# Performance work log

Hardware: AMD Instinct MI355X
Metric: run time of the kernel (lower is better)

The kernel has to match this reference:

```python
import jax, jax.numpy as jnp
import numpy as np

N, C, H, W = 32, 512, 32, 32
K = 64  # num_clusters
D_OUT = 256


def _l2n(v, axis):
    # torch F.normalize: v / max(||v||, 1e-12)
    n = jnp.linalg.norm(v, axis=axis, keepdims=True)
    return v / jnp.maximum(n, 1e-12)


def _bn(v, gamma, beta):
    # BatchNorm1d, training mode (batch stats, biased variance), eps=1e-5
    m = v.mean(axis=0)
    var = ((v - m) ** 2).mean(axis=0)
    return (v - m) / jnp.sqrt(var + 1e-5) * gamma + beta


def setup_inputs() -> dict:
    key = jax.random.key(0)
    ks = jax.random.split(key, 5)
    x = jax.random.normal(ks[0], (N, C, H, W), dtype=jnp.float32)
    conv_w = jax.random.normal(ks[1], (K, C), dtype=jnp.float32) * 0.05
    centroids = jax.random.uniform(ks[2], (K, C), dtype=jnp.float32)
    hidden_w = jax.random.normal(ks[3], (K * C, D_OUT), dtype=jnp.float32) / jnp.sqrt(jnp.float32(C))
    gating_w = jax.random.normal(ks[4], (D_OUT, D_OUT), dtype=jnp.float32) / jnp.sqrt(jnp.float32(D_OUT))
    return {
        "x": x,
        "conv_w": conv_w,
        "centroids": centroids,
        "hidden_w": hidden_w,
        "bn2_gamma": jnp.ones((D_OUT,), jnp.float32),
        "bn2_beta": jnp.zeros((D_OUT,), jnp.float32),
        "gating_w": gating_w,
        "gbn_gamma": jnp.ones((D_OUT,), jnp.float32),
        "gbn_beta": jnp.zeros((D_OUT,), jnp.float32),
    }


def reference(x, conv_w, centroids, hidden_w, bn2_gamma, bn2_beta, gating_w, gbn_gamma, gbn_beta):
    n = x.shape[0]
    # descriptor-wise L2 normalization over channel dim
    x = _l2n(x, axis=1)                                  # [N,C,H,W]
    xf = x.reshape(n, x.shape[1], -1)                    # [N,C,S]
    # 1x1 conv -> soft assignment, softmax over clusters
    sa = jnp.einsum('ncs,kc->nks', xf, conv_w)           # [N,K,S]
    sa = jax.nn.softmax(sa, axis=1)
    # matmul-form NetVLAD: sum_s a[n,k,s]*(x[n,c,s]-cent[k,c])
    vlad = jnp.einsum('nks,ncs->nkc', sa, xf) \
         - sa.sum(axis=-1)[..., None] * centroids[None]  # [N,K,C]
    vlad = _l2n(vlad, axis=2)                            # intra-normalization
    vlad = _l2n(vlad.reshape(n, -1), axis=1)             # [N,K*C]
    v = vlad @ hidden_w                                  # [N,256]
    v = _bn(v, bn2_gamma, bn2_beta)
    # context gating
    gates = jax.nn.sigmoid(_bn(v @ gating_w, gbn_gamma, gbn_beta))
    return v * gates
```

## Files before the change

kernel.cpp:

```cpp
#include <hip/hip_runtime.h>
#include <math.h>

static constexpr int Nb = 32;
static constexpr int Cc = 512;
static constexpr int Ss = 1024;
static constexpr int Kk = 64;
static constexpr int Dd = 256;

typedef __attribute__((ext_vector_type(8))) short bf16x8;
typedef __attribute__((ext_vector_type(4))) float f32x4;
typedef __attribute__((ext_vector_type(4))) unsigned int u32x4;

union FragU { u32x4 u; bf16x8 h; };

__device__ __forceinline__ unsigned hi_pack(float x0, float x1) {
    return __builtin_amdgcn_perm(__float_as_uint(x1), __float_as_uint(x0), 0x07060302u);
}
__device__ __forceinline__ float trunc_hi(float x) {
    return __uint_as_float(__float_as_uint(x) & 0xFFFF0000u);
}
__device__ __forceinline__ void split8(const float* xv, FragU& bh, FragU& bl) {
#pragma unroll
    for (int p = 0; p < 4; ++p) {
        bh.u[p] = hi_pack(xv[2*p], xv[2*p+1]);
        float l0 = xv[2*p]   - trunc_hi(xv[2*p]);
        float l1 = xv[2*p+1] - trunc_hi(xv[2*p+1]);
        bl.u[p] = hi_pack(l0, l1);
    }
}

__global__ __launch_bounds__(256) void kprep_cw(
    const float* __restrict__ cw, short* __restrict__ cwh, short* __restrict__ cwl)
{
    int t = blockIdx.x * 256 + threadIdx.x;
    float4 v = *(const float4*)&cw[4 * (size_t)t];
    unsigned h0 = hi_pack(v.x, v.y), h1 = hi_pack(v.z, v.w);
    float l0 = v.x - trunc_hi(v.x), l1 = v.y - trunc_hi(v.y);
    float l2 = v.z - trunc_hi(v.z), l3 = v.w - trunc_hi(v.w);
    unsigned g0 = hi_pack(l0, l1), g1 = hi_pack(l2, l3);
    ((uint2*)cwh)[t] = make_uint2(h0, h1);
    ((uint2*)cwl)[t] = make_uint2(g0, g1);
}

__global__ __launch_bounds__(512) void k1_sa(
    const float* __restrict__ x, const short* __restrict__ cw_hi,
    const short* __restrict__ cw_lo, short* __restrict__ a_hi,
    short* __restrict__ a_lo, float* __restrict__ asum_part)
{
    __shared__ f32x4 comb[4][64][4];
    __shared__ float combq[4][64];

    const int tid = threadIdx.x;
    const int w = tid >> 6, lane = tid & 63;
    const int wq = w & 3, wh = w >> 2;
    const int l15 = lane & 15, lg = lane >> 4;
    const int n = blockIdx.y, s0 = blockIdx.x * 64;
    const int scol = s0 + 16 * wq + l15;

    f32x4 zero4 = {0.f, 0.f, 0.f, 0.f};
    f32x4 acc[4] = {zero4, zero4, zero4, zero4};
    float ssq = 0.f;

    const float* xcol = x + (size_t)n * Cc * Ss + scol;

#pragma unroll 2
    for (int ct = 0; ct < 8; ++ct) {
        const int cb = wh * 256 + ct * 32 + 8 * lg;
        float xv[8];
#pragma unroll
        for (int j = 0; j < 8; ++j) xv[j] = xcol[(size_t)(cb + j) * Ss];
#pragma unroll
        for (int j = 0; j < 8; ++j) ssq += xv[j] * xv[j];
        FragU bh, bl;
        split8(xv, bh, bl);
#pragma unroll
        for (int m = 0; m < 4; ++m) {
            FragU ah, al;
            const int row = 16 * m + l15;
            ah.u = *(const u32x4*)&cw_hi[(size_t)row * Cc + cb];
            al.u = *(const u32x4*)&cw_lo[(size_t)row * Cc + cb];
            acc[m] = __builtin_amdgcn_mfma_f32_16x16x32_bf16(al.h, bh.h, acc[m], 0, 0, 0);
            acc[m] = __builtin_amdgcn_mfma_f32_16x16x32_bf16(ah.h, bl.h, acc[m], 0, 0, 0);
            acc[m] = __builtin_amdgcn_mfma_f32_16x16x32_bf16(ah.h, bh.h, acc[m], 0, 0, 0);
        }
    }

    if (wh == 1) {
#pragma unroll
        for (int m = 0; m < 4; ++m) comb[wq][lane][m] = acc[m];
        combq[wq][lane] = ssq;
    }
    __syncthreads();
    if (wh == 1) return;

#pragma unroll
    for (int m = 0; m < 4; ++m) acc[m] += comb[wq][lane][m];
    ssq += combq[wq][lane];

    ssq += __shfl_xor(ssq, 16);
    ssq += __shfl_xor(ssq, 32);
    const float inv = 1.f / fmaxf(sqrtf(ssq), 1e-12f);

    float sv[4][4];
    float mmax = -1e30f;
#pragma unroll
    for (int m = 0; m < 4; ++m)
#pragma unroll
        for (int r = 0; r < 4; ++r) {
            sv[m][r] = acc[m][r] * inv;
            mmax = fmaxf(mmax, sv[m][r]);
        }
    mmax = fmaxf(mmax, __shfl_xor(mmax, 16));
    mmax = fmaxf(mmax, __shfl_xor(mmax, 32));
    float den = 0.f;
#pragma unroll
    for (int m = 0; m < 4; ++m)
#pragma unroll
        for (int r = 0; r < 4; ++r) {
            sv[m][r] = expf(sv[m][r] - mmax);
            den += sv[m][r];
        }
    den += __shfl_xor(den, 16);
    den += __shfl_xor(den, 32);
    const float rinv = 1.f / den;

#pragma unroll
    for (int m = 0; m < 4; ++m)
#pragma unroll
        for (int r = 0; r < 4; ++r) {
            const float a = sv[m][r] * rinv;
            const int k = 16 * m + 4 * lg + r;
            float t = a;
            t += __shfl_xor(t, 1); t += __shfl_xor(t, 2);
            t += __shfl_xor(t, 4); t += __shfl_xor(t, 8);
            if (l15 == 0)
                asum_part[((size_t)(n * Kk + k) << 6) + blockIdx.x * 4 + wq] = t;
            const float av = a * inv;
            const unsigned u = __float_as_uint(av);
            const float hv = __uint_as_float(u & 0xFFFF0000u);
            const size_t idx = (size_t)(n * Kk + k) * Ss + scol;
            a_hi[idx] = (short)(u >> 16);
            a_lo[idx] = (short)(__float_as_uint(av - hv) >> 16);
        }
}

__global__ __launch_bounds__(256) void kasum(
    const float* __restrict__ asum_part, float* __restrict__ asum)
{
    int row = blockIdx.x * 256 + threadIdx.x;
    const float* p = &asum_part[(size_t)row << 6];
    float s = 0.f;
#pragma unroll
    for (int i = 0; i < 16; ++i) {
        float4 v = *(const float4*)&p[4 * i];
        s += v.x + v.y + v.z + v.w;
    }
    asum[row] = s;
}

__global__ __launch_bounds__(512) void k2_vlad(
    const float* __restrict__ x, const short* __restrict__ a_hi,
    const short* __restrict__ a_lo, const float* __restrict__ centroids,
    const float* __restrict__ asum, float* __restrict__ vp0,
    float* __restrict__ vp1)
{
    __shared__ f32x4 comb[4][64][4];
    __shared__ float asum_l[64];

    const int tid = threadIdx.x;
    const int w = tid >> 6, lane = tid & 63;
    const int wq = w & 3, wh = w >> 2;
    const int l15 = lane & 15, lg = lane >> 4;
    const int n = blockIdx.x, cp = blockIdx.y, sh = blockIdx.z;

    if (sh == 1 && tid < 64) asum_l[tid] = asum[n * Kk + tid];

    f32x4 zero4 = {0.f, 0.f, 0.f, 0.f};
    f32x4 acc[4] = {zero4, zero4, zero4, zero4};

    const int c = cp * 64 + 16 * wq + l15;
    const int sbase = sh * 512 + wh * 256;
    const float* xrow = x + (size_t)(n * Cc + c) * Ss + sbase;
    const short* ahb = a_hi + (size_t)n * Kk * Ss + sbase;
    const short* alb = a_lo + (size_t)n * Kk * Ss + sbase;

#pragma unroll 2
    for (int st = 0; st < 8; ++st) {
        const int so = st * 32 + 8 * lg;
        float4 xa = *(const float4*)&xrow[so];
        float4 xb = *(const float4*)&xrow[so + 4];
        float xv[8] = {xa.x, xa.y, xa.z, xa.w, xb.x, xb.y, xb.z, xb.w};
        FragU bh, bl;
        split8(xv, bh, bl);
#pragma unroll
        for (int m = 0; m < 4; ++m) {
            FragU ah, al;
            const size_t ao = (size_t)(16 * m + l15) * Ss + so;
            ah.u = *(const u32x4*)&ahb[ao];
            al.u = *(const u32x4*)&alb[ao];
            acc[m] = __builtin_amdgcn_mfma_f32_16x16x32_bf16(al.h, bh.h, acc[m], 0, 0, 0);
            acc[m] = __builtin_amdgcn_mfma_f32_16x16x32_bf16(ah.h, bl.h, acc[m], 0, 0, 0);
            acc[m] = __builtin_amdgcn_mfma_f32_16x16x32_bf16(ah.h, bh.h, acc[m], 0, 0, 0);
        }
    }

    if (wh == 1) {
#pragma unroll
        for (int m = 0; m < 4; ++m) comb[wq][lane][m] = acc[m];
    }
    __syncthreads();
    if (wh == 1) return;

    float* dst = sh ? vp1 : vp0;
#pragma unroll
    for (int m = 0; m < 4; ++m) {
        acc[m] += comb[wq][lane][m];
#pragma unroll
        for (int r = 0; r < 4; ++r) {
            const int k = 16 * m + 4 * lg + r;
            float val = acc[m][r];
            if (sh == 1) val -= asum_l[k] * centroids[(size_t)k * Cc + c];
            dst[(size_t)(n * Kk + k) * Cc + c] = val;
        }
    }
}

__global__ __launch_bounds__(512) void k3a_norm(
    float* __restrict__ vlad, const float* __restrict__ vp1,
    float* __restrict__ nrm)
{
    const int tid = threadIdx.x;
    const int w = tid >> 6, lane = tid & 63;
    const int n = blockIdx.x, kg = blockIdx.y;
    const int row = (n * Kk) + kg * 8 + w;
    const size_t base = (size_t)row * Cc + lane * 8;

    float4 v0 = *(const float4*)&vlad[base];
    float4 v1 = *(const float4*)&vlad[base + 4];
    float4 u0 = *(const float4*)&vp1[base];
    float4 u1 = *(const float4*)&vp1[base + 4];
    v0.x += u0.x; v0.y += u0.y; v0.z += u0.z; v0.w += u0.w;
    v1.x += u1.x; v1.y += u1.y; v1.z += u1.z; v1.w += u1.w;
    *(float4*)&vlad[base] = v0;
    *(float4*)&vlad[base + 4] = v1;
    float ssq = v0.x*v0.x + v0.y*v0.y + v0.z*v0.z + v0.w*v0.w
              + v1.x*v1.x + v1.y*v1.y + v1.z*v1.z + v1.w*v1.w;
#pragma unroll
    for (int off = 32; off >= 1; off >>= 1) ssq += __shfl_xor(ssq, off);
    if (lane == 0) nrm[row] = sqrtf(ssq);
}

__global__ __launch_bounds__(64) void k3b_scale(
    const float* __restrict__ nrm, float* __restrict__ scale)
{
    const int n = blockIdx.x, k = threadIdx.x;
    float r = nrm[n * Kk + k];
    float rn = r / fmaxf(r, 1e-12f);
    float p = rn * rn;
#pragma unroll
    for (int off = 32; off >= 1; off >>= 1) p += __shfl_xor(p, off);
    float g = sqrtf(p);
    scale[n * Kk + k] = 1.f / (fmaxf(r, 1e-12f) * fmaxf(g, 1e-12f));
}

__global__ __launch_bounds__(512) void k4_hidden(
    const float* __restrict__ vlad, const float* __restrict__ scale,
    const float* __restrict__ hw, float* __restrict__ vpart)
{
    __shared__ float vl[128][36];
    __shared__ float scale_l[32];
    const int tid = threadIdx.x;
    const int kc0 = blockIdx.x * 128;
    const int k = kc0 >> 9;
    if (tid < 32) scale_l[tid] = scale[tid * Kk + k];
    __syncthreads();
#pragma unroll
    for (int i = 0; i < 8; ++i) {
        int idx = tid + i * 512;
        int nn = idx >> 7, kcl = idx & 127;
        vl[kcl][nn] = vlad[(size_t)nn * (Kk * Cc) + kc0 + kcl] * scale_l[nn];
    }
    __syncthreads();

    const int dq = tid & 63, nq = tid >> 6;
    float acc[4][4];
#pragma unroll
    for (int i = 0; i < 4; ++i)
#pragma unroll
        for (int j = 0; j < 4; ++j) acc[i][j] = 0.f;

    for (int kcl = 0; kcl < 128; ++kcl) {
        const float4 v0 = *(const float4*)&vl[kcl][nq * 4];
        const float* wrow = &hw[(size_t)(kc0 + kcl) * Dd + dq];
#pragma unroll
        for (int dd = 0; dd < 4; ++dd) {
            float w = wrow[64 * dd];
            acc[dd][0] += w * v0.x; acc[dd][1] += w * v0.y;
            acc[dd][2] += w * v0.z; acc[dd][3] += w * v0.w;
        }
    }
#pragma unroll
    for (int dd = 0; dd < 4; ++dd)
#pragma unroll
        for (int j = 0; j < 4; ++j)
            vpart[((size_t)blockIdx.x * Nb + nq * 4 + j) * Dd + dq + 64 * dd] = acc[dd][j];
}

__global__ __launch_bounds__(128) void k5a_reduce(
    const float* __restrict__ vpart, float* __restrict__ v)
{
    int flat = blockIdx.x * 128 + threadIdx.x;
    float s = 0.f;
#pragma unroll 8
    for (int ch = 0; ch < 256; ++ch) s += vpart[(size_t)ch * (Nb * Dd) + flat];
    v[flat] = s;
}

__global__ __launch_bounds__(256) void k5b_bn(
    const float* __restrict__ v, const float* __restrict__ gamma,
    const float* __restrict__ beta, float* __restrict__ v_bn)
{
    const int d = threadIdx.x;
    float vals[Nb];
    float s1 = 0.f;
#pragma unroll
    for (int n = 0; n < Nb; ++n) {
        vals[n] = v[n * Dd + d];
        s1 += vals[n];
    }
    float m = s1 * (1.f / Nb);
    float var = 0.f;
#pragma unroll
    for (int n = 0; n < Nb; ++n) {
        float t = vals[n] - m;
        var += t * t;
    }
    var *= (1.f / Nb);
    float inv = rsqrtf(var + 1e-5f);
    float g = gamma[d], b = beta[d];
#pragma unroll
    for (int n = 0; n < Nb; ++n)
        v_bn[n * Dd + d] = (vals[n] - m) * inv * g + b;
}

__global__ __launch_bounds__(256) void k5c_gate(
    const float* __restrict__ v_bn, const float* __restrict__ gw,
    float* __restrict__ g_raw)
{
    __shared__ float vb[Dd];
    const int n = blockIdx.x, d = threadIdx.x;
    vb[d] = v_bn[n * Dd + d];
    __syncthreads();
    float acc = 0.f;
#pragma unroll 8
    for (int c = 0; c < Dd; ++c) acc += vb[c] * gw[c * Dd + d];
    g_raw[n * Dd + d] = acc;
}

__global__ __launch_bounds__(256) void k5d_out(
    const float* __restrict__ g_raw, const float* __restrict__ v_bn,
    const float* __restrict__ ggamma, const float* __restrict__ gbeta,
    float* __restrict__ out)
{
    const int d = threadIdx.x;
    float vals[Nb];
    float s1 = 0.f;
#pragma unroll
    for (int n = 0; n < Nb; ++n) {
        vals[n] = g_raw[n * Dd + d];
        s1 += vals[n];
    }
    float m = s1 * (1.f / Nb);
    float var = 0.f;
#pragma unroll
    for (int n = 0; n < Nb; ++n) {
        float t = vals[n] - m;
        var += t * t;
    }
    var *= (1.f / Nb);
    float inv = rsqrtf(var + 1e-5f);
    float g = ggamma[d], b = gbeta[d];
#pragma unroll
    for (int n = 0; n < Nb; ++n) {
        float t = (vals[n] - m) * inv * g + b;
        float sg = 1.f / (1.f + expf(-t));
        out[n * Dd + d] = v_bn[n * Dd + d] * sg;
    }
}

extern "C" void kernel_launch(void* const* d_in, const int* in_sizes, int n_in,
                              void* d_out, int out_size, void* d_ws, size_t ws_size,
                              hipStream_t stream)
{
    const float* x         = (const float*)d_in[0];
    const float* conv_w    = (const float*)d_in[1];
    const float* centroids = (const float*)d_in[2];
    const float* hidden_w  = (const float*)d_in[3];
    const float* bn2_gamma = (const float*)d_in[4];
    const float* bn2_beta  = (const float*)d_in[5];
    const float* gating_w  = (const float*)d_in[6];
    const float* gbn_gamma = (const float*)d_in[7];
    const float* gbn_beta  = (const float*)d_in[8];
    float* out = (float*)d_out;

    char* B = (char*)d_ws;
    short* a_hi      = (short*)(B);
    short* a_lo      = (short*)(B + (4u << 20));
    float* vp0       = (float*)(B + (8u << 20));
    float* vp1       = (float*)(B + (12u << 20));
    short* cw_hi     = (short*)(B + (16u << 20));
    short* cw_lo     = (short*)(B + (16u << 20) + 65536u);
    float* asum_part = (float*)(B + (16u << 20) + 131072u);
    float* asum      = (float*)(B + (16u << 20) + 655360u);
    float* nrm       = asum + 2048;
    float* scale     = nrm + 2048;
    float* v         = scale + 2048;
    float* v_bn      = v + 8192;
    float* g_raw     = v_bn + 8192;
    float* vpart     = (float*)B;

    kprep_cw<<<32, 256, 0, stream>>>(conv_w, cw_hi, cw_lo);
    k1_sa<<<dim3(16, 32), 512, 0, stream>>>(x, cw_hi, cw_lo, a_hi, a_lo, asum_part);
    kasum<<<8, 256, 0, stream>>>(asum_part, asum);
    k2_vlad<<<dim3(32, 8, 2), 512, 0, stream>>>(x, a_hi, a_lo, centroids, asum, vp0, vp1);
    k3a_norm<<<dim3(32, 8), 512, 0, stream>>>(vp0, vp1, nrm);
    k3b_scale<<<32, 64, 0, stream>>>(nrm, scale);
    k4_hidden<<<256, 512, 0, stream>>>(vp0, scale, hidden_w, vpart);
    k5a_reduce<<<64, 128, 0, stream>>>(vpart, v);
    k5b_bn<<<1, 256, 0, stream>>>(v, bn2_gamma, bn2_beta, v_bn);
    k5c_gate<<<32, 256, 0, stream>>>(v_bn, gating_w, g_raw);
    k5d_out<<<1, 256, 0, stream>>>(g_raw, v_bn, gbn_gamma, gbn_beta, out);
}
```

Before: 141.3 us.

## Stage x tiles through double-buffered LDS with float4 loads in soft-assignment kernel

The soft-assignment kernel used to read x straight from global memory as scalar strided loads per column. It now loads 64x64 channel-by-spatial tiles with coalesced float4 reads into a double-buffered shared-memory tile. The next tile is prefetched into registers while MFMAs run on the current one, and the centroid-weight fragments are hoisted ahead of the x reads. The cost is 32KB of extra LDS and a block-wide barrier every iteration, and the channel split between the two wave halves now interleaves within each 64-channel tile.

```diff
diff --git a/kernel.cpp b/kernel.cpp
--- a/kernel.cpp
+++ b/kernel.cpp
@@ -47,6 +47,7 @@
     const short* __restrict__ cw_lo, short* __restrict__ a_hi,
     short* __restrict__ a_lo, float* __restrict__ asum_part)
 {
+    __shared__ float xt[2][64][64];
     __shared__ f32x4 comb[4][64][4];
     __shared__ float combq[4][64];
 
@@ -55,34 +56,62 @@
     const int wq = w & 3, wh = w >> 2;
     const int l15 = lane & 15, lg = lane >> 4;
     const int n = blockIdx.y, s0 = blockIdx.x * 64;
-    const int scol = s0 + 16 * wq + l15;
+
+    const int st_c0 = tid >> 4;
+    const int st_f  = tid & 15;
+    const float* xbase = x + ((size_t)n * Cc) * Ss + s0 + 4 * st_f;
+
+    float4 stv[2];
+    auto GLOAD = [&](int ct) {
+#pragma unroll
+        for (int r = 0; r < 2; ++r)
+            stv[r] = *(const float4*)&xbase[(size_t)(ct * 64 + st_c0 + 32 * r) * Ss];
+    };
+    auto SWRITE = [&](int b) {
+#pragma unroll
+        for (int r = 0; r < 2; ++r)
+            *(float4*)&xt[b][st_c0 + 32 * r][4 * st_f] = stv[r];
+    };
 
     f32x4 zero4 = {0.f, 0.f, 0.f, 0.f};
     f32x4 acc[4] = {zero4, zero4, zero4, zero4};
     float ssq = 0.f;
 
-    const float* xcol = x + (size_t)n * Cc * Ss + scol;
-
-#pragma unroll 2
+    const int sl = 16 * wq + l15;
+    const int cb = wh * 32 + 8 * lg;
+
+    GLOAD(0);
+    SWRITE(0);
+    __syncthreads();
+
     for (int ct = 0; ct < 8; ++ct) {
-        const int cb = wh * 256 + ct * 32 + 8 * lg;
+        if (ct < 7) GLOAD(ct + 1);
+
+        const int b = ct & 1;
+        FragU ah[4], al[4];
+        const int cg = ct * 64 + cb;
+#pragma unroll
+        for (int m = 0; m < 4; ++m) {
+            const int row = 16 * m + l15;
+            ah[m].u = *(const u32x4*)&cw_hi[(size_t)row * Cc + cg];
+            al[m].u = *(const u32x4*)&cw_lo[(size_t)row * Cc + cg];
+        }
         float xv[8];
 #pragma unroll
-        for (int j = 0; j < 8; ++j) xv[j] = xcol[(size_t)(cb + j) * Ss];
+        for (int j = 0; j < 8; ++j) xv[j] = xt[b][cb + j][sl];
 #pragma unroll
         for (int j = 0; j < 8; ++j) ssq += xv[j] * xv[j];
         FragU bh, bl;
         split8(xv, bh, bl);
 #pragma unroll
         for (int m = 0; m < 4; ++m) {
-            FragU ah, al;
-            const int row = 16 * m + l15;
-            ah.u = *(const u32x4*)&cw_hi[(size_t)row * Cc + cb];
-            al.u = *(const u32x4*)&cw_lo[(size_t)row * Cc + cb];
-            acc[m] = __builtin_amdgcn_mfma_f32_16x16x32_bf16(al.h, bh.h, acc[m], 0, 0, 0);
-            acc[m] = __builtin_amdgcn_mfma_f32_16x16x32_bf16(ah.h, bl.h, acc[m], 0, 0, 0);
-            acc[m] = __builtin_amdgcn_mfma_f32_16x16x32_bf16(ah.h, bh.h, acc[m], 0, 0, 0);
-        }
+            acc[m] = __builtin_amdgcn_mfma_f32_16x16x32_bf16(al[m].h, bh.h, acc[m], 0, 0, 0);
+            acc[m] = __builtin_amdgcn_mfma_f32_16x16x32_bf16(ah[m].h, bl.h, acc[m], 0, 0, 0);
+            acc[m] = __builtin_amdgcn_mfma_f32_16x16x32_bf16(ah[m].h, bh.h, acc[m], 0, 0, 0);
+        }
+
+        if (ct < 7) SWRITE((ct + 1) & 1);
+        __syncthreads();
     }
 
     if (wh == 1) {
@@ -124,6 +153,7 @@
     den += __shfl_xor(den, 32);
     const float rinv = 1.f / den;
 
+    const int scol = s0 + sl;
 #pragma unroll
     for (int m = 0; m < 4; ++m)
 #pragma unroll
```

New measurement: 155.2 us. 9.9% more time.

## Stage x tiles through LDS with double-buffered async global-to-LDS loads in k1_sa

Applied to the files above, without the earlier changes.

Reads of the x tile in the soft-assignment kernel now go through shared memory. Each block issues coalesced 16-byte global_load_lds transfers into a double buffer, prefetching the next 64-channel chunk while the MFMAs run on the current one. Previously each lane read strided scalar globals directly. The channel split between the two wave halves changes from contiguous 256-channel halves to interleaved 32-channel slices per chunk. The cost is 32 KB of LDS and a block-wide barrier every iteration, and there is a possible ordering hazard because no explicit vmcnt wait precedes the barrier.

```diff
diff --git a/kernel.cpp b/kernel.cpp
--- a/kernel.cpp
+++ b/kernel.cpp
@@ -27,6 +27,12 @@
         float l1 = xv[2*p+1] - trunc_hi(xv[2*p+1]);
         bl.u[p] = hi_pack(l0, l1);
     }
+}
+
+__device__ __forceinline__ void gload_lds16(const float* g, void* l) {
+    __builtin_amdgcn_global_load_lds(
+        (const __attribute__((address_space(1))) void*)g,
+        (__attribute__((address_space(3))) void*)l, 16, 0, 0);
 }
 
 __global__ __launch_bounds__(256) void kprep_cw(
@@ -47,6 +53,7 @@
     const short* __restrict__ cw_lo, short* __restrict__ a_hi,
     short* __restrict__ a_lo, float* __restrict__ asum_part)
 {
+    __shared__ float xt[2 * 64 * 64];
     __shared__ f32x4 comb[4][64][4];
     __shared__ float combq[4][64];
 
@@ -55,34 +62,53 @@
     const int wq = w & 3, wh = w >> 2;
     const int l15 = lane & 15, lg = lane >> 4;
     const int n = blockIdx.y, s0 = blockIdx.x * 64;
-    const int scol = s0 + 16 * wq + l15;
+
+    const float* xg = x + ((size_t)n * Cc) * Ss + s0 + 4 * (tid & 15);
+    const int st_c = tid >> 4;
+
+    auto GL = [&](int b, int ct) {
+#pragma unroll
+        for (int r = 0; r < 2; ++r) {
+            const float* src = xg + (size_t)(ct * 64 + st_c + 32 * r) * Ss;
+            void* dst = (char*)xt + b * 16384 + 1024 * w + 8192 * r;
+            gload_lds16(src, dst);
+        }
+    };
 
     f32x4 zero4 = {0.f, 0.f, 0.f, 0.f};
     f32x4 acc[4] = {zero4, zero4, zero4, zero4};
     float ssq = 0.f;
 
-    const float* xcol = x + (size_t)n * Cc * Ss + scol;
-
-#pragma unroll 2
+    const int sl = 16 * wq + l15;
+    const int cb = wh * 32 + 8 * lg;
+
+    GL(0, 0);
+    __syncthreads();
+
     for (int ct = 0; ct < 8; ++ct) {
-        const int cb = wh * 256 + ct * 32 + 8 * lg;
+        const int b = ct & 1;
+        if (ct < 7) GL(b ^ 1, ct + 1);
+
         float xv[8];
 #pragma unroll
-        for (int j = 0; j < 8; ++j) xv[j] = xcol[(size_t)(cb + j) * Ss];
+        for (int j = 0; j < 8; ++j) xv[j] = xt[b * 4096 + (cb + j) * 64 + sl];
 #pragma unroll
         for (int j = 0; j < 8; ++j) ssq += xv[j] * xv[j];
         FragU bh, bl;
         split8(xv, bh, bl);
+
+        const int cg = ct * 64 + cb;
 #pragma unroll
         for (int m = 0; m < 4; ++m) {
             FragU ah, al;
             const int row = 16 * m + l15;
-            ah.u = *(const u32x4*)&cw_hi[(size_t)row * Cc + cb];
-            al.u = *(const u32x4*)&cw_lo[(size_t)row * Cc + cb];
+            ah.u = *(const u32x4*)&cw_hi[(size_t)row * Cc + cg];
+            al.u = *(const u32x4*)&cw_lo[(size_t)row * Cc + cg];
             acc[m] = __builtin_amdgcn_mfma_f32_16x16x32_bf16(al.h, bh.h, acc[m], 0, 0, 0);
             acc[m] = __builtin_amdgcn_mfma_f32_16x16x32_bf16(ah.h, bl.h, acc[m], 0, 0, 0);
             acc[m] = __builtin_amdgcn_mfma_f32_16x16x32_bf16(ah.h, bh.h, acc[m], 0, 0, 0);
         }
+        __syncthreads();
     }
 
     if (wh == 1) {
@@ -124,6 +150,7 @@
     den += __shfl_xor(den, 32);
     const float rinv = 1.f / den;
 
+    const int scol = s0 + sl;
 #pragma unroll
     for (int m = 0; m < 4; ++m)
 #pragma unroll
```

Result: no change. 143.6 us (+1.6%).
